# Kernel optimization log

Hardware: AMD Instinct MI355X
Metric: run time of the kernel (lower is better)

Reference implementation:

```python
import jax, jax.numpy as jnp
import numpy as np

D_MODEL = 1024
H = 16
D_K = D_MODEL // H


def setup_inputs() -> dict:
    key = jax.random.key(0)
    ks = jax.random.split(key, 8)
    B, S = 2, 2048
    q = jax.random.normal(ks[0], (B, S, D_MODEL), dtype=jnp.float32)
    k = jax.random.normal(ks[1], (B, S, D_MODEL), dtype=jnp.float32)
    v = jax.random.normal(ks[2], (B, S, D_MODEL), dtype=jnp.float32)
    mask = jnp.ones((B, 1, S), dtype=jnp.int32)  # key-padding mask, 1 = keep
    sc = 1.0 / np.sqrt(D_MODEL)
    # torch Linear weights [out, in]
    Wq = jax.random.normal(ks[3], (D_MODEL, D_MODEL), dtype=jnp.float32) * sc
    Wk = jax.random.normal(ks[4], (D_MODEL, D_MODEL), dtype=jnp.float32) * sc
    Wv = jax.random.normal(ks[5], (D_MODEL, D_MODEL), dtype=jnp.float32) * sc
    Wo = jax.random.normal(ks[6], (D_MODEL, D_MODEL), dtype=jnp.float32) * sc
    return {"q": q, "k": k, "v": v, "mask": mask,
            "Wq": Wq, "Wk": Wk, "Wv": Wv, "Wo": Wo}


def reference(q, k, v, mask, Wq, Wk, Wv, Wo):
    B, Sq, _ = q.shape
    Sk = k.shape[1]
    # projections (torch Linear: x @ W.T), split heads -> [B, H, S, d_k]
    def split_heads(x, W, S):
        return (x @ W.T).reshape(B, S, H, D_K).transpose(0, 2, 1, 3)
    qh = split_heads(q, Wq, Sq)
    kh = split_heads(k, Wk, Sk)
    vh = split_heads(v, Wv, Sk)
    scores = jnp.einsum('bhqd,bhkd->bhqk', qh, kh) / jnp.sqrt(
        jnp.asarray(D_K, qh.dtype))
    # mask.unsqueeze(1): [B,1,S] -> [B,1,1,S]; masked_fill(mask==0, -1e9)
    m = mask[:, None, :, :]
    scores = jnp.where(m == 0, jnp.asarray(-1e9, scores.dtype), scores)
    p = jax.nn.softmax(scores, axis=-1)
    out = jnp.einsum('bhqk,bhkd->bhqd', p, vh)
    out = out.transpose(0, 2, 1, 3).reshape(B, Sq, H * D_K)
    return out @ Wo.T
```

## Files before the change

### kernel.cpp

```cpp
#include <hip/hip_runtime.h>
#include <hip/hip_bf16.h>

#define LOG2E 1.4426950408889634f

typedef __attribute__((ext_vector_type(8))) __bf16 bf16x8;
typedef __attribute__((ext_vector_type(2))) __bf16 bf16x2;
typedef __attribute__((ext_vector_type(4))) float f32x4;
typedef __attribute__((ext_vector_type(16))) float f32x16;

#define MFMA16(a,b,c) __builtin_amdgcn_mfma_f32_16x16x32_bf16((a),(b),(c),0,0,0)
#define MFMA32(a,b,c) __builtin_amdgcn_mfma_f32_32x32x16_bf16((a),(b),(c),0,0,0)

#define GLL16(g, l) __builtin_amdgcn_global_load_lds( \
    (const __attribute__((address_space(1))) void*)(g), \
    (__attribute__((address_space(3))) void*)(l), 16, 0, 0)

__device__ __forceinline__ unsigned short bfu(float f) {
    __bf16 h = (__bf16)f; unsigned short u; __builtin_memcpy(&u, &h, 2); return u;
}
__device__ __forceinline__ unsigned cvtpk(float lo, float hi) {
    bf16x2 t; t.x = (__bf16)lo; t.y = (__bf16)hi;
    unsigned r; __builtin_memcpy(&r, &t, 4); return r;
}
__device__ __forceinline__ bf16x8 pack4(unsigned a, unsigned b, unsigned c, unsigned d) {
    union { unsigned u[4]; bf16x8 v; } t; t.u[0]=a; t.u[1]=b; t.u[2]=c; t.u[3]=d; return t.v;
}
__device__ __forceinline__ bf16x8 cvt8(float4 a, float4 b, float s) {
    bf16x8 o;
    o[0]=(__bf16)(a.x*s); o[1]=(__bf16)(a.y*s); o[2]=(__bf16)(a.z*s); o[3]=(__bf16)(a.w*s);
    o[4]=(__bf16)(b.x*s); o[5]=(__bf16)(b.y*s); o[6]=(__bf16)(b.z*s); o[7]=(__bf16)(b.w*s);
    return o;
}

__global__ __launch_bounds__(256)
void conv_kernel(const float* __restrict__ q, const float* __restrict__ k,
                 const float* __restrict__ v, const float* __restrict__ Wq,
                 const float* __restrict__ Wk, const float* __restrict__ Wv,
                 const float* __restrict__ Wo, unsigned short* __restrict__ Xb,
                 unsigned short* __restrict__ Wb)
{
    const int y = blockIdx.y;
    if (y < 3) {
        const float* s = (y==0)?q:(y==1)?k:v;
        size_t i = ((size_t)blockIdx.x*256 + threadIdx.x)*8;
        float4 a = *(const float4*)(s+i), b = *(const float4*)(s+i+4);
        *(bf16x8*)(Xb + (size_t)y*4194304 + i) = cvt8(a, b, 1.0f);
    } else {
        const int w = blockIdx.x >> 9;
        const float* s = (w==0)?Wq:(w==1)?Wk:(w==2)?Wv:Wo;
        const float sc = (w==0) ? 0.125f*LOG2E : 1.0f;
        size_t i = ((size_t)(blockIdx.x & 511)*256 + threadIdx.x)*8;
        float4 a = *(const float4*)(s+i), b = *(const float4*)(s+i+4);
        *(bf16x8*)(Wb + (size_t)w*1048576 + i) = cvt8(a, b, sc);
    }
}

__global__ __launch_bounds__(256)
void qkv_kernel(const unsigned short* __restrict__ Xb,
                const unsigned short* __restrict__ Wb,
                unsigned short* __restrict__ Qh, unsigned short* __restrict__ Kh,
                unsigned short* __restrict__ Vt)
{
    __shared__ unsigned short As[2][4096];
    __shared__ unsigned short Bs[2][4096];
    const int z = blockIdx.z;
    const unsigned short* X = Xb + (size_t)z*4194304;
    const unsigned short* W = Wb + (size_t)z*1048576;
    const int t = threadIdx.x, wid = t>>6, lane = t&63;
    const int m0 = blockIdx.x*128, n0 = blockIdx.y*128;
    const int wr = (wid>>1)*64, wc = (wid&1)*64;
    const int lr = lane&15, lk = lane>>4;

    f32x4 acc[4][4] = {};

#pragma unroll
    for (int i=0;i<2;++i){
        int flat = i*4096 + wid*1024 + lane*16;
        int row = flat>>6, cb = (flat&63) ^ ((row&3)<<4);
        GLL16(X + (size_t)(m0+row)*1024 + (cb>>1), (char*)&As[0][0] + i*4096 + wid*1024);
        GLL16(W + (size_t)(n0+row)*1024 + (cb>>1), (char*)&Bs[0][0] + i*4096 + wid*1024);
    }
    asm volatile("s_waitcnt vmcnt(0)" ::: "memory");
    __builtin_amdgcn_s_barrier();
    asm volatile("" ::: "memory");

    for (int kt=0; kt<32; ++kt){
        const int cur = kt&1;
        if (kt<31){
            const int nb = cur^1, K0 = (kt+1)*32;
#pragma unroll
            for (int i=0;i<2;++i){
                int flat = i*4096 + wid*1024 + lane*16;
                int row = flat>>6, cb = (flat&63) ^ ((row&3)<<4);
                GLL16(X + (size_t)(m0+row)*1024 + K0 + (cb>>1), (char*)&As[nb][0] + i*4096 + wid*1024);
                GLL16(W + (size_t)(n0+row)*1024 + K0 + (cb>>1), (char*)&Bs[nb][0] + i*4096 + wid*1024);
            }
        }
        bf16x8 a[4], b[4];
#pragma unroll
        for (int i=0;i<4;++i){
            int row = wr+i*16+lr;
            a[i] = *(const bf16x8*)((const char*)&As[cur][0] + row*64 + ((lk*16)^((row&3)<<4)));
        }
#pragma unroll
        for (int j=0;j<4;++j){
            int row = wc+j*16+lr;
            b[j] = *(const bf16x8*)((const char*)&Bs[cur][0] + row*64 + ((lk*16)^((row&3)<<4)));
        }
#pragma unroll
        for (int i=0;i<4;++i)
#pragma unroll
            for (int j=0;j<4;++j)
                acc[i][j] = MFMA16(a[i], b[j], acc[i][j]);
        asm volatile("s_waitcnt vmcnt(0)" ::: "memory");
        __builtin_amdgcn_s_barrier();
        asm volatile("" ::: "memory");
    }

    unsigned short* out = (z==0)?Qh:(z==1)?Kh:Vt;
#pragma unroll
    for (int i=0;i<4;++i)
#pragma unroll
      for (int j=0;j<4;++j)
#pragma unroll
        for (int r=0;r<4;++r){
            int m = m0 + wr + i*16 + lk*4 + r;
            int n = n0 + wc + j*16 + lr;
            int b_ = m>>11, s = m&2047;
            int h = n>>6, d = n&63;
            size_t idx = (z==2) ? ((size_t)(b_*16+h)*64 + d)*2048 + s
                                : ((size_t)(b_*16+h)*2048 + s)*64 + d;
            out[idx] = bfu(acc[i][j][r]);
        }
}

__global__ __launch_bounds__(256)
void oproj_kernel(const unsigned short* __restrict__ Oh,
                  const unsigned short* __restrict__ Wo,
                  float* __restrict__ out)
{
    __shared__ unsigned short As[2][8192];
    __shared__ unsigned short Bs2[2][4096];
    const int t = threadIdx.x, wid = t>>6, lane = t&63;
    const int m0 = blockIdx.x*128, n0 = blockIdx.y*64;
    const int wr = (wid>>1)*64, wc = (wid&1)*32;
    const int lr = lane&15, lk = lane>>4;
    const int fbase = wid*1024 + lane*16;

    f32x4 acc[4][2] = {};

#pragma unroll
    for (int i=0;i<4;++i){
        int flat = i*4096 + fbase, row = flat>>7;
        int cb = (flat&127) ^ ((row&7)<<4);
        int m = m0+row, b_ = m>>11, s = m&2047;
        GLL16(Oh + ((size_t)(b_*16+0)*2048 + s)*64 + (cb>>1), (char*)&As[0][0] + i*4096 + wid*1024);
    }
#pragma unroll
    for (int i=0;i<2;++i){
        int flat = i*4096 + fbase, row = flat>>7;
        int cb = (flat&127) ^ ((row&7)<<4);
        GLL16(Wo + (size_t)(n0+row)*1024 + (cb>>1), (char*)&Bs2[0][0] + i*4096 + wid*1024);
    }

    for (int kt=0; kt<16; ++kt){
        const int cur = kt&1;
        if (kt<15){
            const int nb = cur^1, K0 = (kt+1)*64, h = K0>>6;
#pragma unroll
            for (int i=0;i<4;++i){
                int flat = i*4096 + fbase, row = flat>>7;
                int cb = (flat&127) ^ ((row&7)<<4);
                int m = m0+row, b_ = m>>11, s = m&2047;
                GLL16(Oh + ((size_t)(b_*16+h)*2048 + s)*64 + (cb>>1),
                      (char*)&As[nb][0] + i*4096 + wid*1024);
            }
#pragma unroll
            for (int i=0;i<2;++i){
                int flat = i*4096 + fbase, row = flat>>7;
                int cb = (flat&127) ^ ((row&7)<<4);
                GLL16(Wo + (size_t)(n0+row)*1024 + K0 + (cb>>1),
                      (char*)&Bs2[nb][0] + i*4096 + wid*1024);
            }
            asm volatile("s_waitcnt vmcnt(6)" ::: "memory");
        } else {
            asm volatile("s_waitcnt vmcnt(0)" ::: "memory");
        }
        __builtin_amdgcn_s_barrier();
        asm volatile("" ::: "memory");

        bf16x8 a[4][2], b[2][2];
#pragma unroll
        for (int i=0;i<4;++i){
            int row = wr+i*16+lr, sw = (row&7)<<4;
            const char* rp = (const char*)&As[cur][0] + row*128;
#pragma unroll
            for (int ks=0;ks<2;++ks)
                a[i][ks] = *(const bf16x8*)(rp + ((ks*64 + lk*16)^sw));
        }
#pragma unroll
        for (int j=0;j<2;++j){
            int row = wc+j*16+lr, sw = (row&7)<<4;
            const char* rp = (const char*)&Bs2[cur][0] + row*128;
#pragma unroll
            for (int ks=0;ks<2;++ks)
                b[j][ks] = *(const bf16x8*)(rp + ((ks*64 + lk*16)^sw));
        }
#pragma unroll
        for (int i=0;i<4;++i)
#pragma unroll
          for (int j=0;j<2;++j)
#pragma unroll
            for (int ks=0;ks<2;++ks)
                acc[i][j] = MFMA16(a[i][ks], b[j][ks], acc[i][j]);
        asm volatile("" ::: "memory");
        __builtin_amdgcn_s_barrier();
    }

#pragma unroll
    for (int i=0;i<4;++i)
#pragma unroll
      for (int j=0;j<2;++j)
#pragma unroll
        for (int r=0;r<4;++r){
            int m = m0 + wr + i*16 + lk*4 + r;
            int n = n0 + wc + j*16 + lr;
            out[(size_t)m*1024 + n] = acc[i][j][r];
        }
}

__global__ __launch_bounds__(256)
void attn_kernel(const unsigned short* __restrict__ Qh,
                 const unsigned short* __restrict__ Kh,
                 const unsigned short* __restrict__ Vt,
                 const int* __restrict__ mask,
                 unsigned short* __restrict__ Oh)
{
    __shared__ unsigned short Ks[2][4096];
    __shared__ unsigned short Vs[2][4096];

    const int t = threadIdx.x, wid = t >> 6, lane = t & 63;
    const int l31 = lane & 31, hi = lane >> 5;
    const int linb = blockIdx.x + 16*blockIdx.y;
    const int work = (linb & 7)*64 + (linb >> 3);
    const int bh = work >> 4;
    const int q0 = (work & 15) * 128;
    const int b_ = bh >> 4;
    const int qw = q0 + wid*32 + l31;

    unsigned flagbits;
    {
        const int4* mp = (const int4*)(mask + b_*2048 + (lane&31)*64);
        int bad = 0;
#pragma unroll
        for (int i=0;i<16;++i){ int4 m4 = mp[i];
            bad |= (m4.x==0)|(m4.y==0)|(m4.z==0)|(m4.w==0); }
        unsigned long long bm = __ballot(bad);
        flagbits = (unsigned)bm;
    }

    bf16x8 qf[4];
    const unsigned short* Qp = Qh + ((size_t)bh*2048 + qw)*64 + hi*8;
#pragma unroll
    for (int dc = 0; dc < 4; ++dc) qf[dc] = *(const bf16x8*)(Qp + dc*16);

    const unsigned short* Kbase = Kh + (size_t)bh*2048*64;
    const unsigned short* Vbase = Vt + (size_t)bh*64*2048;

#pragma unroll
    for (int i = 0; i < 2; ++i) {
        int row = wid*16 + i*8 + (lane>>3);
        int g = (lane&7) ^ (row&7);
        GLL16(Kbase + (size_t)row*64 + g*8,  (char*)&Ks[0][0] + (wid*16+i*8)*128);
        GLL16(Vbase + (size_t)row*2048 + g*8, (char*)&Vs[0][0] + (wid*16+i*8)*128);
    }

    f32x16 o0 = {}, o1 = {}, lacc = {};
    f32x16 minit;
#pragma unroll
    for (int r = 0; r < 16; ++r) minit[r] = -12.0f;

    bf16x8 ones;
    { union { unsigned u[4]; bf16x8 v; } tt;
      tt.u[0]=tt.u[1]=tt.u[2]=tt.u[3]=0x3F803F80u; ones = tt.v; }

    const int swz = (l31 & 7) << 3;

    for (int kt = 0; kt < 32; ++kt) {
        const int cur = kt & 1;
        if (kt < 31) {
            const int nb = cur ^ 1;
#pragma unroll
            for (int i = 0; i < 2; ++i) {
                int row = wid*16 + i*8 + (lane>>3);
                int g = (lane&7) ^ (row&7);
                GLL16(Kbase + (size_t)((kt+1)*64 + row)*64 + g*8,  (char*)&Ks[nb][0] + (wid*16+i*8)*128);
                GLL16(Vbase + (size_t)row*2048 + (kt+1)*64 + g*8, (char*)&Vs[nb][0] + (wid*16+i*8)*128);
            }
            asm volatile("s_waitcnt vmcnt(4)" ::: "memory");
        } else {
            asm volatile("s_waitcnt vmcnt(0)" ::: "memory");
        }
        __builtin_amdgcn_s_barrier();
        asm volatile("" ::: "memory");

        const unsigned short* KsB = Ks[cur];
        const unsigned short* VsB = Vs[cur];

        f32x16 s0, s1;
        {
            const unsigned short* kr0 = KsB + (size_t)l31*64;
            const unsigned short* kr1 = KsB + (size_t)(32 + l31)*64;
#pragma unroll
            for (int dc = 0; dc < 4; ++dc) {
                int off = (dc*16 + hi*8) ^ swz;
                bf16x8 k0 = *(const bf16x8*)(kr0 + off);
                bf16x8 k1 = *(const bf16x8*)(kr1 + off);
                if (dc == 0) { s0 = MFMA32(k0, qf[0], minit); s1 = MFMA32(k1, qf[0], minit); }
                else         { s0 = MFMA32(k0, qf[dc], s0);   s1 = MFMA32(k1, qf[dc], s1); }
            }
        }

        bf16x8 vf0[4], vf1[4];
        {
            const unsigned short* vr0 = VsB + (size_t)l31*64;
            const unsigned short* vr1 = VsB + (size_t)(32 + l31)*64;
#pragma unroll
            for (int kc = 0; kc < 4; ++kc) {
                union { unsigned long long q2[2]; bf16x8 v; } a, b;
                int o0u = (kc*16 + 4*hi) ^ swz;
                int o1u = (kc*16 + 8 + 4*hi) ^ swz;
                a.q2[0] = *(const unsigned long long*)(vr0 + o0u);
                a.q2[1] = *(const unsigned long long*)(vr0 + o1u);
                b.q2[0] = *(const unsigned long long*)(vr1 + o0u);
                b.q2[1] = *(const unsigned long long*)(vr1 + o1u);
                vf0[kc] = a.v; vf1[kc] = b.v;
            }
        }

        if (flagbits & (1u << kt)) {
            const int* mrow = mask + b_*2048 + kt*64;
#pragma unroll
            for (int r = 0; r < 16; ++r) {
                int kv = (r&3) + 8*(r>>2) + 4*hi;
                if (mrow[kv] == 0)      s0[r] = -1e9f;
                if (mrow[32 + kv] == 0) s1[r] = -1e9f;
            }
        }

#pragma unroll
        for (int r = 0; r < 16; ++r) {
            s0[r] = __builtin_amdgcn_exp2f(s0[r]);
            s1[r] = __builtin_amdgcn_exp2f(s1[r]);
        }

        bf16x8 pa[4];
        pa[0] = pack4(cvtpk(s0[0],s0[1]),  cvtpk(s0[2],s0[3]),
                      cvtpk(s0[4],s0[5]),  cvtpk(s0[6],s0[7]));
        pa[1] = pack4(cvtpk(s0[8],s0[9]),  cvtpk(s0[10],s0[11]),
                      cvtpk(s0[12],s0[13]),cvtpk(s0[14],s0[15]));
        pa[2] = pack4(cvtpk(s1[0],s1[1]),  cvtpk(s1[2],s1[3]),
                      cvtpk(s1[4],s1[5]),  cvtpk(s1[6],s1[7]));
        pa[3] = pack4(cvtpk(s1[8],s1[9]),  cvtpk(s1[10],s1[11]),
                      cvtpk(s1[12],s1[13]),cvtpk(s1[14],s1[15]));

#pragma unroll
        for (int kc = 0; kc < 4; ++kc) {
            o0 = MFMA32(pa[kc], vf0[kc], o0);
            o1 = MFMA32(pa[kc], vf1[kc], o1);
            lacc = MFMA32(pa[kc], ones, lacc);
        }
        asm volatile("" ::: "memory");
        __builtin_amdgcn_s_barrier();
    }

    unsigned short* Ob = Oh + ((size_t)bh*2048 + q0 + wid*32)*64;
#pragma unroll
    for (int r = 0; r < 16; ++r) {
        int qr = (r&3) + 8*(r>>2) + 4*hi;
        float inv = 1.0f / lacc[r];
        Ob[(size_t)qr*64 + l31]      = bfu(o0[r] * inv);
        Ob[(size_t)qr*64 + 32 + l31] = bfu(o1[r] * inv);
    }
}

extern "C" void kernel_launch(void* const* d_in, const int* in_sizes, int n_in,
                              void* d_out, int out_size, void* d_ws, size_t ws_size,
                              hipStream_t stream)
{
    const float* q  = (const float*)d_in[0];
    const float* k  = (const float*)d_in[1];
    const float* v  = (const float*)d_in[2];
    const int* mask = (const int*)d_in[3];
    const float* Wq = (const float*)d_in[4];
    const float* Wk = (const float*)d_in[5];
    const float* Wv = (const float*)d_in[6];
    const float* Wo = (const float*)d_in[7];
    float* out = (float*)d_out;

    unsigned short* Xb = (unsigned short*)d_ws;
    unsigned short* Wb = Xb + (size_t)12582912;
    unsigned short* Qh = Wb + (size_t)4194304;
    unsigned short* Kh = Qh + (size_t)4194304;
    unsigned short* Vt = Kh + (size_t)4194304;
    unsigned short* Oh = Xb;

    conv_kernel<<<dim3(2048,4), 256, 0, stream>>>(q, k, v, Wq, Wk, Wv, Wo, Xb, Wb);
    qkv_kernel<<<dim3(32,8,3), 256, 0, stream>>>(Xb, Wb, Qh, Kh, Vt);
    attn_kernel<<<dim3(16,32), 256, 0, stream>>>(Qh, Kh, Vt, mask, Oh);
    oproj_kernel<<<dim3(32,16), 256, 0, stream>>>(Oh, Wb + (size_t)3145728, out);
}
```

Baseline: 136.9 us.

## Prepack K/V in fragment order and load attention operands directly to registers

The QKV projection now writes K and V into a layout that matches the per-lane MFMA fragment order, so the attention kernel can fetch each lane's operands straight from global memory as contiguous 16-byte loads. Shared-memory staging, swizzling and the barriers in the attention loop are removed, and a register double-buffer for K tiles replaces them. The goal is to cut LDS traffic and synchronisation. In exchange, every wave now reads K/V from global or L2 on its own instead of sharing tiles within the block, register pressure rises (launch bounds set to 2 blocks), and the scattered stores in the QKV epilogue get more complex.

```diff
diff --git a/kernel.cpp b/kernel.cpp
--- a/kernel.cpp
+++ b/kernel.cpp
@@ -30,6 +30,18 @@
     o[0]=(__bf16)(a.x*s); o[1]=(__bf16)(a.y*s); o[2]=(__bf16)(a.z*s); o[3]=(__bf16)(a.w*s);
     o[4]=(__bf16)(b.x*s); o[5]=(__bf16)(b.y*s); o[6]=(__bf16)(b.z*s); o[7]=(__bf16)(b.w*s);
     return o;
+}
+
+__device__ __forceinline__ size_t kidx(int bh, int s, int d) {
+    int kt = s>>6, half=(s>>5)&1, l31k=s&31;
+    int dc=d>>4, hik=(d>>3)&1, e=d&7;
+    return (((size_t)bh*32+kt)*8 + half*4+dc)*512 + (hik*32+l31k)*8 + e;
+}
+__device__ __forceinline__ size_t vidx(int bh, int s, int d) {
+    int kt=s>>6, kvin=s&63, kc=kvin>>4, rem=kvin&15;
+    int hiv=(rem>>2)&1, e=(rem&3)+4*(rem>>3);
+    int v1=d>>5, l31v=d&31;
+    return (((size_t)bh*32+kt)*8 + kc*2+v1)*512 + (hiv*32+l31v)*8 + e;
 }
 
 __global__ __launch_bounds__(256)
@@ -58,8 +70,8 @@
 __global__ __launch_bounds__(256)
 void qkv_kernel(const unsigned short* __restrict__ Xb,
                 const unsigned short* __restrict__ Wb,
-                unsigned short* __restrict__ Qh, unsigned short* __restrict__ Kh,
-                unsigned short* __restrict__ Vt)
+                unsigned short* __restrict__ Qh, unsigned short* __restrict__ Kg,
+                unsigned short* __restrict__ Vg)
 {
     __shared__ unsigned short As[2][4096];
     __shared__ unsigned short Bs[2][4096];
@@ -117,7 +129,6 @@
         asm volatile("" ::: "memory");
     }
 
-    unsigned short* out = (z==0)?Qh:(z==1)?Kh:Vt;
 #pragma unroll
     for (int i=0;i<4;++i)
 #pragma unroll
@@ -128,9 +139,11 @@
             int n = n0 + wc + j*16 + lr;
             int b_ = m>>11, s = m&2047;
             int h = n>>6, d = n&63;
-            size_t idx = (z==2) ? ((size_t)(b_*16+h)*64 + d)*2048 + s
-                                : ((size_t)(b_*16+h)*2048 + s)*64 + d;
-            out[idx] = bfu(acc[i][j][r]);
+            int bh = b_*16 + h;
+            unsigned short val = bfu(acc[i][j][r]);
+            if (z==0)      Qh[((size_t)bh*2048 + s)*64 + d] = val;
+            else if (z==1) Kg[kidx(bh, s, d)] = val;
+            else           Vg[vidx(bh, s, d)] = val;
         }
 }
 
@@ -229,16 +242,13 @@
         }
 }
 
-__global__ __launch_bounds__(256)
+__global__ __launch_bounds__(256, 2)
 void attn_kernel(const unsigned short* __restrict__ Qh,
-                 const unsigned short* __restrict__ Kh,
-                 const unsigned short* __restrict__ Vt,
+                 const unsigned short* __restrict__ Kg,
+                 const unsigned short* __restrict__ Vg,
                  const int* __restrict__ mask,
                  unsigned short* __restrict__ Oh)
 {
-    __shared__ unsigned short Ks[2][4096];
-    __shared__ unsigned short Vs[2][4096];
-
     const int t = threadIdx.x, wid = t >> 6, lane = t & 63;
     const int l31 = lane & 31, hi = lane >> 5;
     const int linb = blockIdx.x + 16*blockIdx.y;
@@ -264,16 +274,8 @@
 #pragma unroll
     for (int dc = 0; dc < 4; ++dc) qf[dc] = *(const bf16x8*)(Qp + dc*16);
 
-    const unsigned short* Kbase = Kh + (size_t)bh*2048*64;
-    const unsigned short* Vbase = Vt + (size_t)bh*64*2048;
-
-#pragma unroll
-    for (int i = 0; i < 2; ++i) {
-        int row = wid*16 + i*8 + (lane>>3);
-        int g = (lane&7) ^ (row&7);
-        GLL16(Kbase + (size_t)row*64 + g*8,  (char*)&Ks[0][0] + (wid*16+i*8)*128);
-        GLL16(Vbase + (size_t)row*2048 + g*8, (char*)&Vs[0][0] + (wid*16+i*8)*128);
-    }
+    const unsigned short* Kb2 = Kg + (size_t)bh*131072 + lane*8;
+    const unsigned short* Vb2 = Vg + (size_t)bh*131072 + lane*8;
 
     f32x16 o0 = {}, o1 = {}, lacc = {};
     f32x16 minit;
@@ -284,60 +286,23 @@
     { union { unsigned u[4]; bf16x8 v; } tt;
       tt.u[0]=tt.u[1]=tt.u[2]=tt.u[3]=0x3F803F80u; ones = tt.v; }
 
-    const int swz = (l31 & 7) << 3;
-
-    for (int kt = 0; kt < 32; ++kt) {
-        const int cur = kt & 1;
-        if (kt < 31) {
-            const int nb = cur ^ 1;
-#pragma unroll
-            for (int i = 0; i < 2; ++i) {
-                int row = wid*16 + i*8 + (lane>>3);
-                int g = (lane&7) ^ (row&7);
-                GLL16(Kbase + (size_t)((kt+1)*64 + row)*64 + g*8,  (char*)&Ks[nb][0] + (wid*16+i*8)*128);
-                GLL16(Vbase + (size_t)row*2048 + (kt+1)*64 + g*8, (char*)&Vs[nb][0] + (wid*16+i*8)*128);
-            }
-            asm volatile("s_waitcnt vmcnt(4)" ::: "memory");
-        } else {
-            asm volatile("s_waitcnt vmcnt(0)" ::: "memory");
-        }
-        __builtin_amdgcn_s_barrier();
-        asm volatile("" ::: "memory");
-
-        const unsigned short* KsB = Ks[cur];
-        const unsigned short* VsB = Vs[cur];
+    auto KLOAD = [&](bf16x8* kb, int kt) {
+        const unsigned short* p = Kb2 + (size_t)kt*4096;
+#pragma unroll
+        for (int f = 0; f < 8; ++f) kb[f] = *(const bf16x8*)(p + f*512);
+    };
+    auto TILE = [&](const bf16x8* kb, int kt) {
+        bf16x8 vf[8];
+        const unsigned short* vp = Vb2 + (size_t)kt*4096;
+#pragma unroll
+        for (int g = 0; g < 8; ++g) vf[g] = *(const bf16x8*)(vp + g*512);
 
         f32x16 s0, s1;
-        {
-            const unsigned short* kr0 = KsB + (size_t)l31*64;
-            const unsigned short* kr1 = KsB + (size_t)(32 + l31)*64;
-#pragma unroll
-            for (int dc = 0; dc < 4; ++dc) {
-                int off = (dc*16 + hi*8) ^ swz;
-                bf16x8 k0 = *(const bf16x8*)(kr0 + off);
-                bf16x8 k1 = *(const bf16x8*)(kr1 + off);
-                if (dc == 0) { s0 = MFMA32(k0, qf[0], minit); s1 = MFMA32(k1, qf[0], minit); }
-                else         { s0 = MFMA32(k0, qf[dc], s0);   s1 = MFMA32(k1, qf[dc], s1); }
-            }
-        }
-
-        bf16x8 vf0[4], vf1[4];
-        {
-            const unsigned short* vr0 = VsB + (size_t)l31*64;
-            const unsigned short* vr1 = VsB + (size_t)(32 + l31)*64;
-#pragma unroll
-            for (int kc = 0; kc < 4; ++kc) {
-                union { unsigned long long q2[2]; bf16x8 v; } a, b;
-                int o0u = (kc*16 + 4*hi) ^ swz;
-                int o1u = (kc*16 + 8 + 4*hi) ^ swz;
-                a.q2[0] = *(const unsigned long long*)(vr0 + o0u);
-                a.q2[1] = *(const unsigned long long*)(vr0 + o1u);
-                b.q2[0] = *(const unsigned long long*)(vr1 + o0u);
-                b.q2[1] = *(const unsigned long long*)(vr1 + o1u);
-                vf0[kc] = a.v; vf1[kc] = b.v;
-            }
-        }
-
+#pragma unroll
+        for (int dc = 0; dc < 4; ++dc) {
+            if (dc == 0) { s0 = MFMA32(kb[0], qf[0], minit); s1 = MFMA32(kb[4], qf[0], minit); }
+            else         { s0 = MFMA32(kb[dc], qf[dc], s0);  s1 = MFMA32(kb[4+dc], qf[dc], s1); }
+        }
         if (flagbits & (1u << kt)) {
             const int* mrow = mask + b_*2048 + kt*64;
 #pragma unroll
@@ -347,13 +312,11 @@
                 if (mrow[32 + kv] == 0) s1[r] = -1e9f;
             }
         }
-
 #pragma unroll
         for (int r = 0; r < 16; ++r) {
             s0[r] = __builtin_amdgcn_exp2f(s0[r]);
             s1[r] = __builtin_amdgcn_exp2f(s1[r]);
         }
-
         bf16x8 pa[4];
         pa[0] = pack4(cvtpk(s0[0],s0[1]),  cvtpk(s0[2],s0[3]),
                       cvtpk(s0[4],s0[5]),  cvtpk(s0[6],s0[7]));
@@ -363,15 +326,21 @@
                       cvtpk(s1[4],s1[5]),  cvtpk(s1[6],s1[7]));
         pa[3] = pack4(cvtpk(s1[8],s1[9]),  cvtpk(s1[10],s1[11]),
                       cvtpk(s1[12],s1[13]),cvtpk(s1[14],s1[15]));
-
 #pragma unroll
         for (int kc = 0; kc < 4; ++kc) {
-            o0 = MFMA32(pa[kc], vf0[kc], o0);
-            o1 = MFMA32(pa[kc], vf1[kc], o1);
-            lacc = MFMA32(pa[kc], ones, lacc);
-        }
-        asm volatile("" ::: "memory");
-        __builtin_amdgcn_s_barrier();
+            o0   = MFMA32(pa[kc], vf[kc*2],   o0);
+            o1   = MFMA32(pa[kc], vf[kc*2+1], o1);
+            lacc = MFMA32(pa[kc], ones,       lacc);
+        }
+    };
+
+    bf16x8 bufA[8], bufB[8];
+    KLOAD(bufA, 0);
+    for (int kt = 0; kt < 32; kt += 2) {
+        KLOAD(bufB, kt+1);
+        TILE(bufA, kt);
+        if (kt+2 < 32) KLOAD(bufA, kt+2);
+        TILE(bufB, kt+1);
     }
 
     unsigned short* Ob = Oh + ((size_t)bh*2048 + q0 + wid*32)*64;
@@ -401,12 +370,12 @@
     unsigned short* Xb = (unsigned short*)d_ws;
     unsigned short* Wb = Xb + (size_t)12582912;
     unsigned short* Qh = Wb + (size_t)4194304;
-    unsigned short* Kh = Qh + (size_t)4194304;
-    unsigned short* Vt = Kh + (size_t)4194304;
+    unsigned short* Kg = Qh + (size_t)4194304;
+    unsigned short* Vg = Kg + (size_t)4194304;
     unsigned short* Oh = Xb;
 
     conv_kernel<<<dim3(2048,4), 256, 0, stream>>>(q, k, v, Wq, Wk, Wv, Wo, Xb, Wb);
-    qkv_kernel<<<dim3(32,8,3), 256, 0, stream>>>(Xb, Wb, Qh, Kh, Vt);
-    attn_kernel<<<dim3(16,32), 256, 0, stream>>>(Qh, Kh, Vt, mask, Oh);
+    qkv_kernel<<<dim3(32,8,3), 256, 0, stream>>>(Xb, Wb, Qh, Kg, Vg);
+    attn_kernel<<<dim3(16,32), 256, 0, stream>>>(Qh, Kg, Vg, mask, Oh);
     oproj_kernel<<<dim3(32,16), 256, 0, stream>>>(Oh, Wb + (size_t)3145728, out);
 }
```

Result: slower. 146.4 us (+6.9%).
